# Optimization experiments

Hardware: AMD Instinct MI355X
Metric: run time of the kernel (lower is better)

## Reference

```python
import jax, jax.numpy as jnp
import numpy as np

N_NODES = 50000
N_EDGES = 1600000
IN_FEATS = 128
HID = 128
HEADS = 4
F_HEAD = HID // HEADS  # 32
NEG_SLOPE = 0.2


def setup_inputs() -> dict:
    key = jax.random.key(0)
    ks = jax.random.split(key, 7)
    feat = jax.random.normal(ks[0], (N_NODES, IN_FEATS), dtype=jnp.float32)
    # Xavier-ish scaling for the shared fc weight
    W = jax.random.normal(ks[1], (IN_FEATS, HID), dtype=jnp.float32) * (1.0 / np.sqrt(IN_FEATS))
    attn_l = jax.random.normal(ks[2], (HEADS, F_HEAD), dtype=jnp.float32) * 0.1
    attn_r = jax.random.normal(ks[3], (HEADS, F_HEAD), dtype=jnp.float32) * 0.1
    bias = jnp.zeros((HID,), dtype=jnp.float32)
    src_idx = jax.random.randint(ks[4], (N_EDGES,), 0, N_NODES, dtype=jnp.int32)
    dst_idx = jax.random.randint(ks[5], (N_EDGES,), 0, N_NODES, dtype=jnp.int32)
    return {"feat": feat, "W": W, "attn_l": attn_l, "attn_r": attn_r,
            "bias": bias, "src_idx": src_idx, "dst_idx": dst_idx}


def reference(feat, W, attn_l, attn_r, bias, src_idx, dst_idx):
    N = feat.shape[0]
    # shared linear projection, split into heads: [N, H, F]
    ft = (feat @ W).reshape(N, HEADS, F_HEAD)
    # per-node attention logits: [N, H]
    el = jnp.einsum('nhf,hf->nh', ft, attn_l)
    er = jnp.einsum('nhf,hf->nh', ft, attn_r)
    # per-edge unnormalized score: [E, H]
    e = jax.nn.leaky_relu(el[src_idx] + er[dst_idx], negative_slope=NEG_SLOPE)
    # numerically stable edge softmax grouped by destination node
    m = jax.ops.segment_max(e, dst_idx, num_segments=N)          # [N, H]
    m = jnp.where(jnp.isfinite(m), m, 0.0)                       # guard empty dst
    a = jnp.exp(e - m[dst_idx])                                  # [E, H]
    s = jax.ops.segment_sum(a, dst_idx, num_segments=N)          # [N, H]
    alpha = a / jnp.where(s[dst_idx] > 0, s[dst_idx], 1.0)       # [E, H]
    # weighted scatter-sum aggregation: [N, H, F]
    msgs = ft[src_idx] * alpha[:, :, None]
    out = jax.ops.segment_sum(msgs, dst_idx, num_segments=N)
    out = out + bias.reshape(1, HEADS, F_HEAD)
    return out.reshape(N, HEADS * F_HEAD)  # flatten(1)
```

## Files before the change

kernel.cpp:

```cpp
#include <hip/hip_runtime.h>
#include <hip/hip_bf16.h>
#include <math.h>

#define NEG_SLOPE 0.2f
#define NBMAX 1024
#define CAP 4096
#define CH 8192

typedef __attribute__((ext_vector_type(8))) short short8;
typedef __attribute__((ext_vector_type(4))) float f32x4;
typedef __attribute__((ext_vector_type(2))) float f32x2;
union BU { uint4 u; short8 s; };

__device__ __forceinline__ unsigned bf16rne(float f) {
    unsigned u = __float_as_uint(f);
    return (u + 0x7fffu + ((u >> 16) & 1u)) >> 16;
}
__device__ __forceinline__ short bf16s(float f) { return (short)bf16rne(f); }

__global__ __launch_bounds__(256) void k_wprep(
    const float* __restrict__ W, const float* __restrict__ attn_l,
    const float* __restrict__ attn_r, uint4* __restrict__ Wfrag,
    float4* __restrict__ WL, float4* __restrict__ WR,
    int* __restrict__ gcur, int NB) {
    int tid = blockIdx.x * 256 + threadIdx.x;
    if (tid < 2048) {
        int lane = tid & 63;
        int ki = (tid >> 6) & 3;
        int t = (tid >> 8) & 3;
        int cg = tid >> 10;
        int col = cg * 64 + t * 16 + (lane & 15);
        int kb = ki * 32 + (lane >> 4) * 8;
        unsigned d[4];
#pragma unroll
        for (int p = 0; p < 4; ++p) {
            unsigned lo = bf16rne(W[(kb + 2 * p) * 128 + col]);
            unsigned hi = bf16rne(W[(kb + 2 * p + 1) * 128 + col]);
            d[p] = lo | (hi << 16);
        }
        Wfrag[tid] = make_uint4(d[0], d[1], d[2], d[3]);
    } else if (tid < 2048 + 128) {
        int k = tid - 2048;
        const float* wr_ = W + k * 128;
        float l0 = 0, l1 = 0, l2 = 0, l3 = 0, r0 = 0, r1 = 0, r2 = 0, r3 = 0;
        for (int j = 0; j < 32; ++j) {
            l0 += wr_[j] * attn_l[j];
            l1 += wr_[32 + j] * attn_l[32 + j];
            l2 += wr_[64 + j] * attn_l[64 + j];
            l3 += wr_[96 + j] * attn_l[96 + j];
            r0 += wr_[j] * attn_r[j];
            r1 += wr_[32 + j] * attn_r[32 + j];
            r2 += wr_[64 + j] * attn_r[64 + j];
            r3 += wr_[96 + j] * attn_r[96 + j];
        }
        WL[k] = make_float4(l0, l1, l2, l3);
        WR[k] = make_float4(r0, r1, r2, r3);
    } else if (tid - 2176 < NB) {
        gcur[tid - 2176] = 0;
    }
}

__global__ __launch_bounds__(256) void k_fc(
    const float* __restrict__ feat, const uint4* __restrict__ Wfrag,
    const f32x4* __restrict__ WL, const f32x4* __restrict__ WR,
    unsigned* __restrict__ ftbf, float* __restrict__ el, float* __restrict__ er,
    int N) {
    __shared__ f32x4 WLs[128], WRs[128];
    int tid = threadIdx.x;
    if (tid < 128) WLs[tid] = WL[tid];
    else WRs[tid - 128] = WR[tid - 128];
    __syncthreads();
    const int wave = tid >> 6, lane = tid & 63;
    const int rt = wave & 1, cg = wave >> 1;
    const int nbase = blockIdx.x * 32 + rt * 16;
    const int row = nbase + (lane & 15);
    const int rowc = min(row, N - 1);
    const int q = lane >> 4;

    BU b[4][4];
#pragma unroll
    for (int t = 0; t < 4; ++t)
#pragma unroll
        for (int ki = 0; ki < 4; ++ki)
            b[t][ki].u = Wfrag[cg * 1024 + t * 256 + ki * 64 + lane];

    f32x4 acc0 = {0, 0, 0, 0}, acc1 = {0, 0, 0, 0}, acc2 = {0, 0, 0, 0}, acc3 = {0, 0, 0, 0};
    f32x4 elacc = {0, 0, 0, 0}, eracc = {0, 0, 0, 0};
    const float* fr = feat + (size_t)rowc * 128;
#pragma unroll
    for (int ki = 0; ki < 4; ++ki) {
        float4 f0 = *(const float4*)(fr + ki * 32 + q * 8);
        float4 f1 = *(const float4*)(fr + ki * 32 + q * 8 + 4);
        short8 a;
        a[0] = bf16s(f0.x); a[1] = bf16s(f0.y); a[2] = bf16s(f0.z); a[3] = bf16s(f0.w);
        a[4] = bf16s(f1.x); a[5] = bf16s(f1.y); a[6] = bf16s(f1.z); a[7] = bf16s(f1.w);
        acc0 = __builtin_amdgcn_mfma_f32_16x16x32_bf16(a, b[0][ki].s, acc0, 0, 0, 0);
        acc1 = __builtin_amdgcn_mfma_f32_16x16x32_bf16(a, b[1][ki].s, acc1, 0, 0, 0);
        acc2 = __builtin_amdgcn_mfma_f32_16x16x32_bf16(a, b[2][ki].s, acc2, 0, 0, 0);
        acc3 = __builtin_amdgcn_mfma_f32_16x16x32_bf16(a, b[3][ki].s, acc3, 0, 0, 0);
        if (cg == 0) {
            int kb = ki * 32 + q * 8;
            elacc += f0.x * WLs[kb + 0]; eracc += f0.x * WRs[kb + 0];
            elacc += f0.y * WLs[kb + 1]; eracc += f0.y * WRs[kb + 1];
            elacc += f0.z * WLs[kb + 2]; eracc += f0.z * WRs[kb + 2];
            elacc += f0.w * WLs[kb + 3]; eracc += f0.w * WRs[kb + 3];
            elacc += f1.x * WLs[kb + 4]; eracc += f1.x * WRs[kb + 4];
            elacc += f1.y * WLs[kb + 5]; eracc += f1.y * WRs[kb + 5];
            elacc += f1.z * WLs[kb + 6]; eracc += f1.z * WRs[kb + 6];
            elacc += f1.w * WLs[kb + 7]; eracc += f1.w * WRs[kb + 7];
        }
    }
#pragma unroll
    for (int t = 0; t < 4; ++t) {
#pragma unroll
        for (int r = 0; r < 4; ++r) {
            float d = (t == 0) ? acc0[r] : (t == 1) ? acc1[r] : (t == 2) ? acc2[r] : acc3[r];
            unsigned m = bf16rne(d);
            unsigned nb = (unsigned)__shfl_xor((int)m, 1, 64);
            int node = nbase + q * 4 + r;
            if (!(lane & 1) && node < N)
                ftbf[(size_t)node * 64 + cg * 32 + t * 8 + ((lane & 15) >> 1)] = m | (nb << 16);
        }
    }
    if (cg == 0) {
#pragma unroll
        for (int c = 0; c < 4; ++c) {
            elacc[c] += __shfl_xor(elacc[c], 16, 64);
            eracc[c] += __shfl_xor(eracc[c], 16, 64);
            elacc[c] += __shfl_xor(elacc[c], 32, 64);
            eracc[c] += __shfl_xor(eracc[c], 32, 64);
        }
        if (lane < 16 && row < N) {
            *(float4*)(el + (size_t)row * 4) = make_float4(elacc[0], elacc[1], elacc[2], elacc[3]);
            *(float4*)(er + (size_t)row * 4) = make_float4(eracc[0], eracc[1], eracc[2], eracc[3]);
        }
    }
}

__global__ __launch_bounds__(1024) void k_scatter_b(
    const int* __restrict__ src, const int* __restrict__ dst,
    int* __restrict__ gcur, unsigned* __restrict__ B, int E, int NB) {
    __shared__ int h[NBMAX];
    __shared__ int lc[NBMAX];
    __shared__ int dl[CH];
    int tid = threadIdx.x;
    for (int t = tid; t < NB; t += 1024) h[t] = 0;
    __syncthreads();
    int beg = blockIdx.x * CH;
    int end = min(beg + CH, E);
    for (int i = beg + tid; i < end; i += 1024) {
        int d = dst[i];
        dl[i - beg] = d;
        atomicAdd(&h[d >> 6], 1);
    }
    __syncthreads();
    for (int t = tid; t < NB; t += 1024)
        lc[t] = (h[t] > 0) ? atomicAdd(&gcur[t], h[t]) : 0;
    __syncthreads();
    for (int i = beg + tid; i < end; i += 1024) {
        int d = dl[i - beg];
        int pos = atomicAdd(&lc[d >> 6], 1);
        if (pos < CAP)
            B[(size_t)(d >> 6) * CAP + pos] = ((unsigned)src[i] << 6) | (unsigned)(d & 63);
    }
}

__global__ __launch_bounds__(512) void k_sort(
    const unsigned* __restrict__ B, const int* __restrict__ gcur,
    int* __restrict__ srt, uint2* __restrict__ od, int N) {
    __shared__ int hist[64];
    __shared__ int cur[64];
    const int tid = threadIdx.x;
    const int b = blockIdx.x;
    const int m = min(gcur[b], CAP);
    const size_t base = (size_t)b * CAP;
    if (tid < 64) hist[tid] = 0;
    __syncthreads();
    for (int i = tid; i < m; i += 512) atomicAdd(&hist[B[base + i] & 63], 1);
    __syncthreads();
    int v0 = (tid < 64) ? hist[tid] : 0;
    for (int off = 1; off < 64; off <<= 1) {
        int t = (tid < 64 && tid >= off) ? hist[tid - off] : 0;
        __syncthreads();
        if (tid < 64) hist[tid] += t;
        __syncthreads();
    }
    if (tid < 64) {
        int ex = hist[tid] - v0;
        cur[tid] = ex;
        int node = (b << 6) + tid;
        if (node < N) od[node] = make_uint2((unsigned)(base + ex), (unsigned)v0);
    }
    __syncthreads();
    for (int i = tid; i < m; i += 512) {
        unsigned p = B[base + i];
        int pos = atomicAdd(&cur[p & 63], 1);
        srt[base + pos] = (int)(p >> 6);
    }
}

__global__ __launch_bounds__(256, 8) void k_aggregate(
    const unsigned* __restrict__ ftbf, const float* __restrict__ el,
    const float* __restrict__ er, const int* __restrict__ srt,
    const uint2* __restrict__ od, const float* __restrict__ bias,
    float* __restrict__ out, int N) {
    __shared__ float als[4][64][4];
    __shared__ int snl[4][64];
    const int wave = threadIdx.x >> 6;
    const int lane = threadIdx.x & 63;
    const int l15 = lane & 15;
    const int hd = l15 >> 2;
    const int g = lane >> 4;
    int node = blockIdx.x * 4 + wave;
    if (node >= N) return;
    uint2 o = od[node];
    int beg = (int)o.x, cnt = (int)o.y;
    float4 erd = *(const float4*)(er + (size_t)node * 4);
    const uint4* ftv = (const uint4*)ftbf;

    float s0 = 0.f, s1 = 0.f, s2 = 0.f, s3 = 0.f;
    f32x2 p0 = {0, 0}, p1 = {0, 0}, p2 = {0, 0}, p3 = {0, 0};
    for (int tile = 0; tile < cnt; tile += 64) {
        int tc = min(64, cnt - tile);
        int tcm1 = tc - 1;
        float a0 = 0.f, a1 = 0.f, a2 = 0.f, a3 = 0.f;
        int sn = 0;
        if (lane < tc) {
            sn = srt[beg + tile + lane];
            float4 a = *(const float4*)(el + (size_t)sn * 4);
            float e0 = a.x + erd.x; e0 = fmaxf(e0, NEG_SLOPE * e0);
            float e1 = a.y + erd.y; e1 = fmaxf(e1, NEG_SLOPE * e1);
            float e2 = a.z + erd.z; e2 = fmaxf(e2, NEG_SLOPE * e2);
            float e3 = a.w + erd.w; e3 = fmaxf(e3, NEG_SLOPE * e3);
            a0 = __expf(e0); a1 = __expf(e1);
            a2 = __expf(e2); a3 = __expf(e3);
        }
        s0 += a0; s1 += a1; s2 += a2; s3 += a3;
        *(float4*)(&als[wave][lane][0]) = make_float4(a0, a1, a2, a3);
        snl[wave][lane] = sn;
        int sA = snl[wave][min(g, tcm1)];
        int sB = snl[wave][min(4 + g, tcm1)];
        uint4 uA = ftv[((size_t)sA << 4) + l15];
        uint4 uB = ftv[((size_t)sB << 4) + l15];
        for (int jj0 = 0; jj0 < tc; jj0 += 8) {
            float afA = (jj0 + g < tc) ? als[wave][jj0 + g][hd] : 0.f;
            float afB = (jj0 + 4 + g < tc) ? als[wave][jj0 + 4 + g][hd] : 0.f;
            uint4 vA = uA, vB = uB;
            if (jj0 + 8 < tc) {
                int s = snl[wave][min(jj0 + 8 + g, tcm1)];
                uA = ftv[((size_t)s << 4) + l15];
            }
            if (jj0 + 12 < tc) {
                int s = snl[wave][min(jj0 + 12 + g, tcm1)];
                uB = ftv[((size_t)s << 4) + l15];
            }
            {
                f32x2 af2 = {afA, afA};
                p0 += (f32x2){__uint_as_float(vA.x << 16), __uint_as_float(vA.x & 0xffff0000u)} * af2;
                p1 += (f32x2){__uint_as_float(vA.y << 16), __uint_as_float(vA.y & 0xffff0000u)} * af2;
                p2 += (f32x2){__uint_as_float(vA.z << 16), __uint_as_float(vA.z & 0xffff0000u)} * af2;
                p3 += (f32x2){__uint_as_float(vA.w << 16), __uint_as_float(vA.w & 0xffff0000u)} * af2;
            }
            {
                f32x2 af2 = {afB, afB};
                p0 += (f32x2){__uint_as_float(vB.x << 16), __uint_as_float(vB.x & 0xffff0000u)} * af2;
                p1 += (f32x2){__uint_as_float(vB.y << 16), __uint_as_float(vB.y & 0xffff0000u)} * af2;
                p2 += (f32x2){__uint_as_float(vB.z << 16), __uint_as_float(vB.z & 0xffff0000u)} * af2;
                p3 += (f32x2){__uint_as_float(vB.w << 16), __uint_as_float(vB.w & 0xffff0000u)} * af2;
            }
        }
    }
#pragma unroll
    for (int off = 16; off <= 32; off <<= 1) {
        p0.x += __shfl_xor(p0.x, off, 64); p0.y += __shfl_xor(p0.y, off, 64);
        p1.x += __shfl_xor(p1.x, off, 64); p1.y += __shfl_xor(p1.y, off, 64);
        p2.x += __shfl_xor(p2.x, off, 64); p2.y += __shfl_xor(p2.y, off, 64);
        p3.x += __shfl_xor(p3.x, off, 64); p3.y += __shfl_xor(p3.y, off, 64);
    }
#pragma unroll
    for (int off = 32; off >= 1; off >>= 1) {
        s0 += __shfl_xor(s0, off, 64);
        s1 += __shfl_xor(s1, off, 64);
        s2 += __shfl_xor(s2, off, 64);
        s3 += __shfl_xor(s3, off, 64);
    }
    float ssel = (hd == 0) ? s0 : (hd == 1) ? s1 : (hd == 2) ? s2 : s3;
    float inv = ssel > 0.f ? 1.f / ssel : 0.f;
    if (lane < 16) {
        int c0 = lane * 8;
        float4 b0 = *(const float4*)(bias + c0);
        float4 b1 = *(const float4*)(bias + c0 + 4);
        float4 o0, o1;
        o0.x = p0.x * inv + b0.x; o0.y = p0.y * inv + b0.y;
        o0.z = p1.x * inv + b0.z; o0.w = p1.y * inv + b0.w;
        o1.x = p2.x * inv + b1.x; o1.y = p2.y * inv + b1.y;
        o1.z = p3.x * inv + b1.z; o1.w = p3.y * inv + b1.w;
        *(float4*)(out + (size_t)node * 128 + c0) = o0;
        *(float4*)(out + (size_t)node * 128 + c0 + 4) = o1;
    }
}

extern "C" void kernel_launch(void* const* d_in, const int* in_sizes, int n_in,
                              void* d_out, int out_size, void* d_ws, size_t ws_size,
                              hipStream_t stream) {
    const float* feat = (const float*)d_in[0];
    const float* W = (const float*)d_in[1];
    const float* attn_l = (const float*)d_in[2];
    const float* attn_r = (const float*)d_in[3];
    const float* bias = (const float*)d_in[4];
    const int* src = (const int*)d_in[5];
    const int* dst = (const int*)d_in[6];
    const int N = in_sizes[0] / 128;
    const int E = in_sizes[5];
    const int NB = (N + 63) >> 6;
    float* out = (float*)d_out;

    char* p = (char*)d_ws;
    unsigned int* ftbf = (unsigned int*)p;  p += (size_t)N * 64 * 4;
    unsigned* B = (unsigned*)p;             p += (size_t)NB * CAP * 4;
    int* srt = (int*)p;                     p += (size_t)NB * CAP * 4;
    float* el = (float*)p;                  p += (size_t)N * 4 * 4;
    float* er = (float*)p;                  p += (size_t)N * 4 * 4;
    uint2* od = (uint2*)p;                  p += (size_t)N * 8;
    int* gcur = (int*)p;                    p += ((size_t)NB * 4 + 15) & ~15ull;
    uint4* Wfrag = (uint4*)p;               p += 2048 * 16;
    float4* WL = (float4*)p;                p += 128 * 16;
    float4* WR = (float4*)p;                p += 128 * 16;

    int eblocks = (E + CH - 1) / CH;
    k_wprep<<<12, 256, 0, stream>>>(W, attn_l, attn_r, Wfrag, WL, WR, gcur, NB);
    k_fc<<<(N + 31) / 32, 256, 0, stream>>>(feat, Wfrag, (const f32x4*)WL,
                                            (const f32x4*)WR, ftbf, el, er, N);
    k_scatter_b<<<eblocks, 1024, 0, stream>>>(src, dst, gcur, B, E, NB);
    k_sort<<<NB, 512, 0, stream>>>(B, gcur, srt, od, N);
    k_aggregate<<<(N + 3) / 4, 256, 0, stream>>>(ftbf, el, er, srt, od, bias, out, N);
}
```

Baseline: 111.3 us.

## Split aggregation per head with head-major features and precomputed fp16 edge weights

The feature table is stored head-major, so each head's 32 bf16 columns are contiguous across nodes. The sort kernel now computes the unnormalized attention weight per edge and packs it as fp16 together with a 16-bit source index, padding each node's edge list to a multiple of 16. Aggregation runs as a separate pass per head, gathering 64-byte rows so each pass works on a smaller, more cache-friendly slice. The costs are fp16 weight precision, a source index that only fits below 65536 nodes, four times the packed-edge traffic, and lower bucket capacities that could drop edges for skewed degree distributions.

Result: slower. 187.1 us (+68.1%).

```diff
diff --git a/kernel.cpp b/kernel.cpp
--- a/kernel.cpp
+++ b/kernel.cpp
@@ -1,10 +1,12 @@
 #include <hip/hip_runtime.h>
 #include <hip/hip_bf16.h>
+#include <hip/hip_fp16.h>
 #include <math.h>
 
 #define NEG_SLOPE 0.2f
 #define NBMAX 1024
-#define CAP 4096
+#define CAP_E 2560
+#define CAP_P 3584
 #define CH 8192
 
 typedef __attribute__((ext_vector_type(8))) short short8;
@@ -118,8 +120,10 @@
             unsigned m = bf16rne(d);
             unsigned nb = (unsigned)__shfl_xor((int)m, 1, 64);
             int node = nbase + q * 4 + r;
+            int cp = cg * 32 + t * 8 + ((lane & 15) >> 1);
             if (!(lane & 1) && node < N)
-                ftbf[(size_t)node * 64 + cg * 32 + t * 8 + ((lane & 15) >> 1)] = m | (nb << 16);
+                ftbf[(size_t)(cp >> 4) * ((size_t)N * 16) + (size_t)node * 16 + (cp & 15)]
+                    = m | (nb << 16);
         }
     }
     if (cg == 0) {
@@ -160,25 +164,36 @@
     for (int i = beg + tid; i < end; i += 1024) {
         int d = dl[i - beg];
         int pos = atomicAdd(&lc[d >> 6], 1);
-        if (pos < CAP)
-            B[(size_t)(d >> 6) * CAP + pos] = ((unsigned)src[i] << 6) | (unsigned)(d & 63);
-    }
-}
-
-__global__ __launch_bounds__(512) void k_sort(
+        if (pos < CAP_E)
+            B[(size_t)(d >> 6) * CAP_E + pos] = ((unsigned)src[i] << 6) | (unsigned)(d & 63);
+    }
+}
+
+__global__ __launch_bounds__(256) void k_sortalpha(
     const unsigned* __restrict__ B, const int* __restrict__ gcur,
-    int* __restrict__ srt, uint2* __restrict__ od, int N) {
+    const float* __restrict__ el, const float* __restrict__ er,
+    unsigned* __restrict__ apk, uint2* __restrict__ od,
+    int N, int S) {
     __shared__ int hist[64];
     __shared__ int cur[64];
+    __shared__ int pexс[64];
+    __shared__ int pv0[64];
     const int tid = threadIdx.x;
     const int b = blockIdx.x;
-    const int m = min(gcur[b], CAP);
-    const size_t base = (size_t)b * CAP;
+    const int m = min(gcur[b], CAP_E);
+    const size_t baseE = (size_t)b * CAP_E;
+    const size_t baseP = (size_t)b * CAP_P;
     if (tid < 64) hist[tid] = 0;
     __syncthreads();
-    for (int i = tid; i < m; i += 512) atomicAdd(&hist[B[base + i] & 63], 1);
-    __syncthreads();
-    int v0 = (tid < 64) ? hist[tid] : 0;
+    for (int i = tid; i < m; i += 256) atomicAdd(&hist[B[baseE + i] & 63], 1);
+    __syncthreads();
+    int v0 = 0, pc = 0;
+    if (tid < 64) {
+        v0 = hist[tid];
+        pc = (v0 + 15) & ~15;
+        hist[tid] = pc;
+    }
+    __syncthreads();
     for (int off = 1; off < 64; off <<= 1) {
         int t = (tid < 64 && tid >= off) ? hist[tid - off] : 0;
         __syncthreads();
@@ -186,108 +201,100 @@
         __syncthreads();
     }
     if (tid < 64) {
-        int ex = hist[tid] - v0;
+        int ex = hist[tid] - pc;
         cur[tid] = ex;
+        pexс[tid] = ex;
+        pv0[tid] = v0;
         int node = (b << 6) + tid;
-        if (node < N) od[node] = make_uint2((unsigned)(base + ex), (unsigned)v0);
-    }
-    __syncthreads();
-    for (int i = tid; i < m; i += 512) {
-        unsigned p = B[base + i];
-        int pos = atomicAdd(&cur[p & 63], 1);
-        srt[base + pos] = (int)(p >> 6);
-    }
-}
-
-__global__ __launch_bounds__(256, 8) void k_aggregate(
-    const unsigned* __restrict__ ftbf, const float* __restrict__ el,
-    const float* __restrict__ er, const int* __restrict__ srt,
+        if (node < N) od[node] = make_uint2((unsigned)(baseP + ex), (unsigned)pc);
+    }
+    __syncthreads();
+    for (int i = tid; i < m; i += 256) {
+        unsigned p = B[baseE + i];
+        int d = (int)(p & 63u);
+        int sn = (int)(p >> 6);
+        float4 a = *(const float4*)(el + (size_t)sn * 4);
+        float4 bb = *(const float4*)(er + (size_t)((b << 6) + d) * 4);
+        float e0 = a.x + bb.x; e0 = fmaxf(e0, NEG_SLOPE * e0);
+        float e1 = a.y + bb.y; e1 = fmaxf(e1, NEG_SLOPE * e1);
+        float e2 = a.z + bb.z; e2 = fmaxf(e2, NEG_SLOPE * e2);
+        float e3 = a.w + bb.w; e3 = fmaxf(e3, NEG_SLOPE * e3);
+        unsigned h0 = __half_as_ushort(__float2half(__expf(e0)));
+        unsigned h1 = __half_as_ushort(__float2half(__expf(e1)));
+        unsigned h2 = __half_as_ushort(__float2half(__expf(e2)));
+        unsigned h3 = __half_as_ushort(__float2half(__expf(e3)));
+        int pos = atomicAdd(&cur[d], 1);
+        unsigned s16 = (unsigned)sn << 16;
+        size_t ix = baseP + (size_t)pos;
+        apk[ix] = s16 | h0;
+        apk[(size_t)S + ix] = s16 | h1;
+        apk[(size_t)2 * S + ix] = s16 | h2;
+        apk[(size_t)3 * S + ix] = s16 | h3;
+    }
+    __syncthreads();
+    if (tid < 64) {
+        int ex = pexс[tid];
+        int vv = pv0[tid];
+        int pcn = (vv + 15) & ~15;
+        for (int j = ex + vv; j < ex + pcn; ++j) {
+            size_t ix = baseP + (size_t)j;
+            apk[ix] = 0u;
+            apk[(size_t)S + ix] = 0u;
+            apk[(size_t)2 * S + ix] = 0u;
+            apk[(size_t)3 * S + ix] = 0u;
+        }
+    }
+}
+
+__global__ __launch_bounds__(256) void k_headpass(
+    const unsigned* __restrict__ ftbf, const unsigned* __restrict__ apk,
     const uint2* __restrict__ od, const float* __restrict__ bias,
-    float* __restrict__ out, int N) {
-    __shared__ float als[4][64][4];
-    __shared__ int snl[4][64];
+    float* __restrict__ out, int N, int S, int NBK) {
+    __shared__ unsigned snl[4][64];
+    const int h = blockIdx.x / NBK;
+    const int nb = blockIdx.x % NBK;
     const int wave = threadIdx.x >> 6;
     const int lane = threadIdx.x & 63;
-    const int l15 = lane & 15;
-    const int hd = l15 >> 2;
-    const int g = lane >> 4;
-    int node = blockIdx.x * 4 + wave;
+    const int node = nb * 4 + wave;
     if (node >= N) return;
     uint2 o = od[node];
-    int beg = (int)o.x, cnt = (int)o.y;
-    float4 erd = *(const float4*)(er + (size_t)node * 4);
-    const uint4* ftv = (const uint4*)ftbf;
-
-    float s0 = 0.f, s1 = 0.f, s2 = 0.f, s3 = 0.f;
+    const unsigned* ah = apk + (size_t)h * S;
+    int off = (int)o.x, pcnt = (int)o.y;
+    const uint4* ftv = (const uint4*)(ftbf) + (size_t)h * N * 4 + (lane & 3);
+
+    float s = 0.f;
     f32x2 p0 = {0, 0}, p1 = {0, 0}, p2 = {0, 0}, p3 = {0, 0};
-    for (int tile = 0; tile < cnt; tile += 64) {
-        int tc = min(64, cnt - tile);
-        int tcm1 = tc - 1;
-        float a0 = 0.f, a1 = 0.f, a2 = 0.f, a3 = 0.f;
-        int sn = 0;
-        if (lane < tc) {
-            sn = srt[beg + tile + lane];
-            float4 a = *(const float4*)(el + (size_t)sn * 4);
-            float e0 = a.x + erd.x; e0 = fmaxf(e0, NEG_SLOPE * e0);
-            float e1 = a.y + erd.y; e1 = fmaxf(e1, NEG_SLOPE * e1);
-            float e2 = a.z + erd.z; e2 = fmaxf(e2, NEG_SLOPE * e2);
-            float e3 = a.w + erd.w; e3 = fmaxf(e3, NEG_SLOPE * e3);
-            a0 = __expf(e0); a1 = __expf(e1);
-            a2 = __expf(e2); a3 = __expf(e3);
-        }
-        s0 += a0; s1 += a1; s2 += a2; s3 += a3;
-        *(float4*)(&als[wave][lane][0]) = make_float4(a0, a1, a2, a3);
-        snl[wave][lane] = sn;
-        int sA = snl[wave][min(g, tcm1)];
-        int sB = snl[wave][min(4 + g, tcm1)];
-        uint4 uA = ftv[((size_t)sA << 4) + l15];
-        uint4 uB = ftv[((size_t)sB << 4) + l15];
-        for (int jj0 = 0; jj0 < tc; jj0 += 8) {
-            float afA = (jj0 + g < tc) ? als[wave][jj0 + g][hd] : 0.f;
-            float afB = (jj0 + 4 + g < tc) ? als[wave][jj0 + 4 + g][hd] : 0.f;
-            uint4 vA = uA, vB = uB;
-            if (jj0 + 8 < tc) {
-                int s = snl[wave][min(jj0 + 8 + g, tcm1)];
-                uA = ftv[((size_t)s << 4) + l15];
-            }
-            if (jj0 + 12 < tc) {
-                int s = snl[wave][min(jj0 + 12 + g, tcm1)];
-                uB = ftv[((size_t)s << 4) + l15];
-            }
-            {
-                f32x2 af2 = {afA, afA};
-                p0 += (f32x2){__uint_as_float(vA.x << 16), __uint_as_float(vA.x & 0xffff0000u)} * af2;
-                p1 += (f32x2){__uint_as_float(vA.y << 16), __uint_as_float(vA.y & 0xffff0000u)} * af2;
-                p2 += (f32x2){__uint_as_float(vA.z << 16), __uint_as_float(vA.z & 0xffff0000u)} * af2;
-                p3 += (f32x2){__uint_as_float(vA.w << 16), __uint_as_float(vA.w & 0xffff0000u)} * af2;
-            }
-            {
-                f32x2 af2 = {afB, afB};
-                p0 += (f32x2){__uint_as_float(vB.x << 16), __uint_as_float(vB.x & 0xffff0000u)} * af2;
-                p1 += (f32x2){__uint_as_float(vB.y << 16), __uint_as_float(vB.y & 0xffff0000u)} * af2;
-                p2 += (f32x2){__uint_as_float(vB.z << 16), __uint_as_float(vB.z & 0xffff0000u)} * af2;
-                p3 += (f32x2){__uint_as_float(vB.w << 16), __uint_as_float(vB.w & 0xffff0000u)} * af2;
-            }
-        }
-    }
-#pragma unroll
-    for (int off = 16; off <= 32; off <<= 1) {
-        p0.x += __shfl_xor(p0.x, off, 64); p0.y += __shfl_xor(p0.y, off, 64);
-        p1.x += __shfl_xor(p1.x, off, 64); p1.y += __shfl_xor(p1.y, off, 64);
-        p2.x += __shfl_xor(p2.x, off, 64); p2.y += __shfl_xor(p2.y, off, 64);
-        p3.x += __shfl_xor(p3.x, off, 64); p3.y += __shfl_xor(p3.y, off, 64);
-    }
-#pragma unroll
-    for (int off = 32; off >= 1; off >>= 1) {
-        s0 += __shfl_xor(s0, off, 64);
-        s1 += __shfl_xor(s1, off, 64);
-        s2 += __shfl_xor(s2, off, 64);
-        s3 += __shfl_xor(s3, off, 64);
-    }
-    float ssel = (hd == 0) ? s0 : (hd == 1) ? s1 : (hd == 2) ? s2 : s3;
-    float inv = ssel > 0.f ? 1.f / ssel : 0.f;
-    if (lane < 16) {
-        int c0 = lane * 8;
+    for (int tile = 0; tile < pcnt; tile += 64) {
+        int tc = min(64, pcnt - tile);
+        unsigned rec = 0;
+        if (lane < tc) rec = ah[(size_t)off + tile + lane];
+        s += __half2float(__ushort_as_half((unsigned short)(rec & 0xffffu)));
+        snl[wave][lane] = rec;
+        int it = tc >> 4;
+        for (int i = 0; i < it; ++i) {
+            unsigned r2 = snl[wave][(i << 4) + (lane >> 2)];
+            float a = __half2float(__ushort_as_half((unsigned short)(r2 & 0xffffu)));
+            int sn = (int)(r2 >> 16);
+            uint4 u = ftv[(size_t)sn * 4];
+            f32x2 a2 = {a, a};
+            p0 += (f32x2){__uint_as_float(u.x << 16), __uint_as_float(u.x & 0xffff0000u)} * a2;
+            p1 += (f32x2){__uint_as_float(u.y << 16), __uint_as_float(u.y & 0xffff0000u)} * a2;
+            p2 += (f32x2){__uint_as_float(u.z << 16), __uint_as_float(u.z & 0xffff0000u)} * a2;
+            p3 += (f32x2){__uint_as_float(u.w << 16), __uint_as_float(u.w & 0xffff0000u)} * a2;
+        }
+    }
+#pragma unroll
+    for (int off2 = 4; off2 <= 32; off2 <<= 1) {
+        p0.x += __shfl_xor(p0.x, off2, 64); p0.y += __shfl_xor(p0.y, off2, 64);
+        p1.x += __shfl_xor(p1.x, off2, 64); p1.y += __shfl_xor(p1.y, off2, 64);
+        p2.x += __shfl_xor(p2.x, off2, 64); p2.y += __shfl_xor(p2.y, off2, 64);
+        p3.x += __shfl_xor(p3.x, off2, 64); p3.y += __shfl_xor(p3.y, off2, 64);
+    }
+#pragma unroll
+    for (int off2 = 1; off2 <= 32; off2 <<= 1) s += __shfl_xor(s, off2, 64);
+    float inv = s > 0.f ? 1.f / s : 0.f;
+    if (lane < 4) {
+        int c0 = h * 32 + lane * 8;
         float4 b0 = *(const float4*)(bias + c0);
         float4 b1 = *(const float4*)(bias + c0 + 4);
         float4 o0, o1;
@@ -313,12 +320,14 @@
     const int N = in_sizes[0] / 128;
     const int E = in_sizes[5];
     const int NB = (N + 63) >> 6;
+    const int S = NB * CAP_P;
+    const int NBK = (N + 3) / 4;
     float* out = (float*)d_out;
 
     char* p = (char*)d_ws;
     unsigned int* ftbf = (unsigned int*)p;  p += (size_t)N * 64 * 4;
-    unsigned* B = (unsigned*)p;             p += (size_t)NB * CAP * 4;
-    int* srt = (int*)p;                     p += (size_t)NB * CAP * 4;
+    unsigned* apk = (unsigned*)p;           p += (size_t)4 * S * 4;
+    unsigned* B = (unsigned*)p;             p += ((size_t)NB * CAP_E * 4 + 15) & ~15ull;
     float* el = (float*)p;                  p += (size_t)N * 4 * 4;
     float* er = (float*)p;                  p += (size_t)N * 4 * 4;
     uint2* od = (uint2*)p;                  p += (size_t)N * 8;
@@ -332,6 +341,6 @@
     k_fc<<<(N + 31) / 32, 256, 0, stream>>>(feat, Wfrag, (const f32x4*)WL,
                                             (const f32x4*)WR, ftbf, el, er, N);
     k_scatter_b<<<eblocks, 1024, 0, stream>>>(src, dst, gcur, B, E, NB);
-    k_sort<<<NB, 512, 0, stream>>>(B, gcur, srt, od, N);
-    k_aggregate<<<(N + 3) / 4, 256, 0, stream>>>(ftbf, el, er, srt, od, bias, out, N);
-}
+    k_sortalpha<<<NB, 256, 0, stream>>>(B, gcur, el, er, apk, od, N, S);
+    k_headpass<<<4 * NBK, 256, 0, stream>>>(ftbf, apk, od, bias, out, N, S, NBK);
+}
```
